# Performance work log

Measured on AMD Instinct MI355X. Metric: run time of the kernel, lower is better.

## Reference

```python
import jax, jax.numpy as jnp
import numpy as np

BEV_H, BEV_W, BEV_Z = 128, 128, 16
N_VOX = BEV_H * BEV_W * BEV_Z  # 262144
C = 128
N_UNMASKED = N_VOX // 4       # 65536 seed voxels (proposal > 0)
LN_EPS = 1e-5
NEG_SLOPE = 0.01


def setup_inputs() -> dict:
    key = jax.random.key(0)
    ks = jax.random.split(key, 8)
    x3d = jax.random.normal(ks[0], (1, C, N_VOX), dtype=jnp.float32)
    # disjoint unmasked/masked index sets from a permutation (proposal mask)
    perm = jax.random.permutation(ks[1], N_VOX)
    unmasked_idx = jnp.sort(perm[:N_UNMASKED]).astype(jnp.int32)
    masked_idx = jnp.sort(perm[N_UNMASKED:]).astype(jnp.int32)
    s = 0.05
    return {
        "x3d": x3d,
        "w1": jax.random.normal(ks[2], (C, C // 2), jnp.float32) * s,
        "b1": jnp.zeros((C // 2,), jnp.float32),
        "ln_g": jnp.ones((C // 2,), jnp.float32),
        "ln_b": jnp.zeros((C // 2,), jnp.float32),
        "w2": jax.random.normal(ks[3], (C // 2, C), jnp.float32) * s,
        "b2": jnp.zeros((C,), jnp.float32),
        "sdb_w": jax.random.normal(ks[4], (C, C // 2), jnp.float32) * s,
        "sdb_b": jnp.zeros((C // 2,), jnp.float32),
        "ssc_w": jax.random.normal(ks[5], (C // 2, 20), jnp.float32) * s,
        "ssc_b": jnp.zeros((20,), jnp.float32),
        "aux_w": jax.random.normal(ks[6], (C, 20), jnp.float32) * s,
        "aux_b": jnp.zeros((20,), jnp.float32),
        "unmasked_idx": unmasked_idx,
        "masked_idx": masked_idx,
    }


def _leaky(x):
    return jnp.where(x > 0, x, NEG_SLOPE * x)


def _layernorm(x, g, b):
    mu = jnp.mean(x, axis=-1, keepdims=True)
    var = jnp.mean(jnp.square(x - mu), axis=-1, keepdims=True)
    return (x - mu) * jax.lax.rsqrt(var + LN_EPS) * g + b


def reference(x3d, w1, b1, ln_g, ln_b, w2, b2, sdb_w, sdb_b, ssc_w, ssc_b,
              aux_w, aux_b, unmasked_idx, masked_idx):
    feats = x3d[0].T  # [N_vox, C]
    # gather seed (unmasked) voxel features; SGB treated as identity stand-in
    seed_feats = feats[unmasked_idx]            # [Nu, C]
    # gather masked voxel features and infill with mlp_prior:
    # Linear -> LayerNorm -> LeakyReLU -> Linear
    m = feats[masked_idx]                       # [Nm, C]
    h = _leaky(_layernorm(m @ w1 + b1, ln_g, ln_b))
    prior = h @ w2 + b2                         # [Nm, C]
    # scatter both into the dense voxel grid
    vox = jnp.zeros((N_VOX, C), x3d.dtype)
    vox = vox.at[unmasked_idx].set(seed_feats).at[masked_idx].set(prior)
    # SDB dense decode stand-in: pointwise conv C -> C/2 + LeakyReLU
    d = _leaky(vox @ sdb_w + sdb_b)             # [N_vox, C/2]
    # ssc head: per-voxel logits -> [1, 20, H, W, Z]
    ssc = d @ ssc_w + ssc_b                     # [N_vox, 20]
    ssc_logit = ssc.reshape(BEV_H, BEV_W, BEV_Z, 20).transpose(3, 0, 1, 2)[None]
    # aux sparse head on seed features
    sem_logit = seed_feats @ aux_w + aux_b      # [Nu, 20]
    return ssc_logit, sem_logit
```

## Files before the change

kernel.cpp:

```cpp
#include <hip/hip_runtime.h>
#include <hip/hip_bf16.h>


#define NVOX 262144
#define NU   65536
#define NM   196608
#define CIN  128
#define CHALF 64
#define NCLS 20
#define TR   64
#define NBLK_M (NM / TR)
#define NBLK_U (NU / TR)

#define SXS 136
#define SHS 72

#define W1F  0
#define W2F  8192
#define SDBF 16384
#define SSCF 24576
#define AUXF 26624
#define WS_TOT 30720

typedef unsigned short u16;
typedef short    bf16x8 __attribute__((ext_vector_type(8)));
typedef float    f32x4  __attribute__((ext_vector_type(4)));

__device__ __forceinline__ u16 f2b(float f) {
    __hip_bfloat16 h = __float2bfloat16(f);
    return *(u16*)&h;
}

__global__ void prep_weights(const float* __restrict__ w1,  const float* __restrict__ w2,
                             const float* __restrict__ sdbw,const float* __restrict__ sscw,
                             const float* __restrict__ auxw,u16* __restrict__ ws) {
    int i = blockIdx.x * blockDim.x + threadIdx.x;
    const int stride = gridDim.x * blockDim.x;
    for (; i < WS_TOT; i += stride) {
        float v;
        if (i < W2F) {
            int t = i, j = t & 7, lane = (t >> 3) & 63, kc = (t >> 9) & 3, nt = t >> 11;
            int k = kc*32 + (lane >> 4)*8 + j, n = nt*16 + (lane & 15);
            v = w1[k*CHALF + n];
        } else if (i < SDBF) {
            int t = i - W2F, j = t & 7, lane = (t >> 3) & 63, kc = (t >> 9) & 1, nt = t >> 10;
            int k = kc*32 + (lane >> 4)*8 + j, n = nt*16 + (lane & 15);
            v = w2[k*CIN + n];
        } else if (i < SSCF) {
            int t = i - SDBF, j = t & 7, lane = (t >> 3) & 63, kc = (t >> 9) & 3, nt = t >> 11;
            int k = kc*32 + (lane >> 4)*8 + j, n = nt*16 + (lane & 15);
            v = sdbw[k*CHALF + n];
        } else if (i < AUXF) {
            int t = i - SSCF, j = t & 7, lane = (t >> 3) & 63, kc = (t >> 9) & 1, nt = t >> 10;
            int k = kc*32 + (lane >> 4)*8 + j, n = nt*16 + (lane & 15);
            v = (n < NCLS) ? sscw[k*NCLS + n] : 0.f;
        } else {
            int t = i - AUXF, j = t & 7, lane = (t >> 3) & 63, kc = (t >> 9) & 3, nt = t >> 11;
            int k = kc*32 + (lane >> 4)*8 + j, n = nt*16 + (lane & 15);
            v = (n < NCLS) ? auxw[k*NCLS + n] : 0.f;
        }
        ws[i] = f2b(v);
    }
}

__global__ __launch_bounds__(256, 3)
void sgn_mfma(const float* __restrict__ x3d,
              const float* __restrict__ b1,   const float* __restrict__ lng,
              const float* __restrict__ lnb,  const float* __restrict__ bb2,
              const float* __restrict__ sdbb, const float* __restrict__ sscb,
              const float* __restrict__ auxb,
              const int* __restrict__ uidx,   const int* __restrict__ midx,
              const u16* __restrict__ wt,     float* __restrict__ out)
{
    __shared__ __align__(16) u16 sX[TR * SXS];
    __shared__ __align__(16) u16 sH[TR * SHS];
    __shared__ __align__(16) u16 wbuf[8192];
    __shared__ int sN[TR];

    const int tid = threadIdx.x;
    const bool masked = (blockIdx.x < NBLK_M);
    const int p0 = (masked ? (int)blockIdx.x : ((int)blockIdx.x - NBLK_M)) * TR;
    const int* __restrict__ idx = masked ? midx : uidx;

    const int r   = tid & 63;
    const int n_r = idx[p0 + r];
    if (tid < TR) sN[tid] = n_r;

    const int cb = (tid >> 6) * 32;
    float v[32];
    #pragma unroll
    for (int j = 0; j < 32; ++j)
        v[j] = x3d[(size_t)(cb + j) * NVOX + n_r];

    {
        const uint4* src = (const uint4*)(wt + (masked ? W1F : SDBF));
        #pragma unroll
        for (int t = 0; t < 4; ++t)
            ((uint4*)wbuf)[tid + t*256] = src[tid + t*256];
    }

    #pragma unroll
    for (int ch = 0; ch < 4; ++ch) {
        bf16x8 pk;
        #pragma unroll
        for (int j = 0; j < 8; ++j) ((u16*)&pk)[j] = f2b(v[ch*8 + j]);
        *(bf16x8*)&sX[r * SXS + cb + ch*8] = pk;
    }
    __syncthreads();

    const int m0   = (tid >> 6) * 16;
    const int lane = tid & 63;
    const int q    = lane >> 4;
    const int n15  = lane & 15;
    const int kq   = q * 8;

    if (masked) {
        f32x4 acc[4];
        #pragma unroll
        for (int nt = 0; nt < 4; ++nt) {
            const float b = b1[nt*16 + n15];
            acc[nt] = (f32x4){b, b, b, b};
        }
        #pragma unroll
        for (int kc = 0; kc < 4; ++kc) {
            const bf16x8 a = *(const bf16x8*)&sX[(m0 + n15) * SXS + kc*32 + kq];
            #pragma unroll
            for (int nt = 0; nt < 4; ++nt) {
                const bf16x8 b = *(const bf16x8*)&wbuf[((nt*4 + kc)*64 + lane)*8];
                acc[nt] = __builtin_amdgcn_mfma_f32_16x16x32_bf16(a, b, acc[nt], 0, 0, 0);
            }
        }
        {
            float gv[4], ev[4];
            #pragma unroll
            for (int nt = 0; nt < 4; ++nt) { gv[nt] = lng[nt*16 + n15]; ev[nt] = lnb[nt*16 + n15]; }
            #pragma unroll
            for (int reg = 0; reg < 4; ++reg) {
                float s1 = acc[0][reg] + acc[1][reg] + acc[2][reg] + acc[3][reg];
                float s2 = acc[0][reg]*acc[0][reg] + acc[1][reg]*acc[1][reg]
                         + acc[2][reg]*acc[2][reg] + acc[3][reg]*acc[3][reg];
                #pragma unroll
                for (int m = 1; m <= 8; m <<= 1) {
                    s1 += __shfl_xor(s1, m, 64);
                    s2 += __shfl_xor(s2, m, 64);
                }
                const float mu  = s1 * (1.f/64.f);
                const float var = s2 * (1.f/64.f) - mu*mu;
                const float rs  = rsqrtf(var + 1e-5f);
                #pragma unroll
                for (int nt = 0; nt < 4; ++nt) {
                    float h = (acc[nt][reg] - mu) * rs * gv[nt] + ev[nt];
                    h = h > 0.f ? h : 0.01f*h;
                    sH[(m0 + q*4 + reg) * SHS + nt*16 + n15] = f2b(h);
                }
            }
        }
        __syncthreads();

        #pragma unroll
        for (int t = 0; t < 4; ++t)
            ((uint4*)wbuf)[tid + t*256] = ((const uint4*)(wt + W2F))[tid + t*256];
        __syncthreads();

        f32x4 acc2[8];
        #pragma unroll
        for (int nt = 0; nt < 8; ++nt) {
            const float b = bb2[nt*16 + n15];
            acc2[nt] = (f32x4){b, b, b, b};
        }
        #pragma unroll
        for (int kc = 0; kc < 2; ++kc) {
            const bf16x8 a = *(const bf16x8*)&sH[(m0 + n15) * SHS + kc*32 + kq];
            #pragma unroll
            for (int nt = 0; nt < 8; ++nt) {
                const bf16x8 b = *(const bf16x8*)&wbuf[((nt*2 + kc)*64 + lane)*8];
                acc2[nt] = __builtin_amdgcn_mfma_f32_16x16x32_bf16(a, b, acc2[nt], 0, 0, 0);
            }
        }
        #pragma unroll
        for (int reg = 0; reg < 4; ++reg)
            #pragma unroll
            for (int nt = 0; nt < 8; ++nt)
                sX[(m0 + q*4 + reg) * SXS + nt*16 + n15] = f2b(acc2[nt][reg]);
        __syncthreads();

        #pragma unroll
        for (int t = 0; t < 4; ++t)
            ((uint4*)wbuf)[tid + t*256] = ((const uint4*)(wt + SDBF))[tid + t*256];
        __syncthreads();
    }

    {
        f32x4 accd[4];
        #pragma unroll
        for (int nt = 0; nt < 4; ++nt) {
            const float b = sdbb[nt*16 + n15];
            accd[nt] = (f32x4){b, b, b, b};
        }
        #pragma unroll
        for (int kc = 0; kc < 4; ++kc) {
            const bf16x8 a = *(const bf16x8*)&sX[(m0 + n15) * SXS + kc*32 + kq];
            #pragma unroll
            for (int nt = 0; nt < 4; ++nt) {
                const bf16x8 b = *(const bf16x8*)&wbuf[((nt*4 + kc)*64 + lane)*8];
                accd[nt] = __builtin_amdgcn_mfma_f32_16x16x32_bf16(a, b, accd[nt], 0, 0, 0);
            }
        }
        #pragma unroll
        for (int reg = 0; reg < 4; ++reg)
            #pragma unroll
            for (int nt = 0; nt < 4; ++nt) {
                float vv = accd[nt][reg];
                vv = vv > 0.f ? vv : 0.01f*vv;
                sH[(m0 + q*4 + reg) * SHS + nt*16 + n15] = f2b(vv);
            }
    }
    __syncthreads();

    if (masked) {
        if (tid < 256) ((uint4*)wbuf)[tid] = ((const uint4*)(wt + SSCF))[tid];
    } else {
        #pragma unroll
        for (int t = 0; t < 3; ++t)
            ((uint4*)wbuf)[tid + t*256] = ((const uint4*)(wt + SSCF))[tid + t*256];
    }
    __syncthreads();

    {
        f32x4 accs[2];
        #pragma unroll
        for (int nt = 0; nt < 2; ++nt) {
            const int col = nt*16 + n15;
            const float b = (col < NCLS) ? sscb[col] : 0.f;
            accs[nt] = (f32x4){b, b, b, b};
        }
        #pragma unroll
        for (int kc = 0; kc < 2; ++kc) {
            const bf16x8 a = *(const bf16x8*)&sH[(m0 + n15) * SHS + kc*32 + kq];
            #pragma unroll
            for (int nt = 0; nt < 2; ++nt) {
                const bf16x8 b = *(const bf16x8*)&wbuf[((nt*2 + kc)*64 + lane)*8];
                accs[nt] = __builtin_amdgcn_mfma_f32_16x16x32_bf16(a, b, accs[nt], 0, 0, 0);
            }
        }
        int ng[4];
        #pragma unroll
        for (int reg = 0; reg < 4; ++reg) ng[reg] = sN[m0 + q*4 + reg];
        #pragma unroll
        for (int reg = 0; reg < 4; ++reg)
            out[(size_t)n15 * NVOX + ng[reg]] = accs[0][reg];
        if (n15 < 4) {
            #pragma unroll
            for (int reg = 0; reg < 4; ++reg)
                out[(size_t)(16 + n15) * NVOX + ng[reg]] = accs[1][reg];
        }
    }

    if (!masked) {
        f32x4 acca[2];
        #pragma unroll
        for (int nt = 0; nt < 2; ++nt) {
            const int col = nt*16 + n15;
            const float b = (col < NCLS) ? auxb[col] : 0.f;
            acca[nt] = (f32x4){b, b, b, b};
        }
        #pragma unroll
        for (int kc = 0; kc < 4; ++kc) {
            const bf16x8 a = *(const bf16x8*)&sX[(m0 + n15) * SXS + kc*32 + kq];
            #pragma unroll
            for (int nt = 0; nt < 2; ++nt) {
                const bf16x8 b = *(const bf16x8*)&wbuf[2048 + ((nt*4 + kc)*64 + lane)*8];
                acca[nt] = __builtin_amdgcn_mfma_f32_16x16x32_bf16(a, b, acca[nt], 0, 0, 0);
            }
        }
        const size_t base = (size_t)NCLS * NVOX;
        #pragma unroll
        for (int reg = 0; reg < 4; ++reg) {
            const int u = p0 + m0 + q*4 + reg;
            out[base + (size_t)u * NCLS + n15] = acca[0][reg];
            if (n15 < 4)
                out[base + (size_t)u * NCLS + 16 + n15] = acca[1][reg];
        }
    }
}

extern "C" void kernel_launch(void* const* d_in, const int* in_sizes, int n_in,
                              void* d_out, int out_size, void* d_ws, size_t ws_size,
                              hipStream_t stream) {
    const float* x3d  = (const float*)d_in[0];
    const float* w1   = (const float*)d_in[1];
    const float* b1   = (const float*)d_in[2];
    const float* lng  = (const float*)d_in[3];
    const float* lnb  = (const float*)d_in[4];
    const float* w2   = (const float*)d_in[5];
    const float* bb2  = (const float*)d_in[6];
    const float* sdbw = (const float*)d_in[7];
    const float* sdbb = (const float*)d_in[8];
    const float* sscw = (const float*)d_in[9];
    const float* sscb = (const float*)d_in[10];
    const float* auxw = (const float*)d_in[11];
    const float* auxb = (const float*)d_in[12];
    const int*   uidx = (const int*)d_in[13];
    const int*   midx = (const int*)d_in[14];
    float* out = (float*)d_out;
    u16*   wt  = (u16*)d_ws;

    hipLaunchKernelGGL(prep_weights, dim3(64), dim3(256), 0, stream,
                       w1, w2, sdbw, sscw, auxw, wt);
    hipLaunchKernelGGL(sgn_mfma, dim3(NBLK_M + NBLK_U), dim3(256), 0, stream,
                       x3d, b1, lng, lnb, bb2, sdbb, sscb, auxb,
                       uidx, midx, wt, out);
}
```

Measured before the change: 263.9 us.

## Process voxels in grid order with a rank map instead of gathering by index

Instead of gathering masked and unmasked voxels through index lists, which makes every x3d read and ssc write strided, each block now takes 64 consecutive voxels. A rank map built in the prep kernel marks each voxel as a seed (its rank) or masked (-1). All voxels run the prior MLP and only masked rows overwrite their features. ssc outputs go through shared memory for coalesced stores. This trades extra MLP and aux compute on every voxel, plus a rank scatter in prep, for fully coalesced vectorized global loads and stores.

```diff
diff --git a/kernel.cpp b/kernel.cpp
--- a/kernel.cpp
+++ b/kernel.cpp
@@ -9,8 +9,7 @@
 #define CHALF 64
 #define NCLS 20
 #define TR   64
-#define NBLK_M (NM / TR)
-#define NBLK_U (NU / TR)
+#define NBLK (NVOX / TR)
 
 #define SXS 136
 #define SHS 72
@@ -20,7 +19,7 @@
 #define SDBF 16384
 #define SSCF 24576
 #define AUXF 26624
-#define WS_TOT 30720
+#define WS_WT 30720
 
 typedef unsigned short u16;
 typedef short    bf16x8 __attribute__((ext_vector_type(8)));
@@ -33,10 +32,15 @@
 
 __global__ void prep_weights(const float* __restrict__ w1,  const float* __restrict__ w2,
                              const float* __restrict__ sdbw,const float* __restrict__ sscw,
-                             const float* __restrict__ auxw,u16* __restrict__ ws) {
+                             const float* __restrict__ auxw,
+                             const int* __restrict__ uidx,  const int* __restrict__ midx,
+                             u16* __restrict__ ws) {
     int i = blockIdx.x * blockDim.x + threadIdx.x;
     const int stride = gridDim.x * blockDim.x;
-    for (; i < WS_TOT; i += stride) {
+    int* __restrict__ rank = (int*)(ws + WS_WT);
+    for (int t = i; t < NU; t += stride) rank[uidx[t]] = t;
+    for (int t = i; t < NM; t += stride) rank[midx[t]] = -1;
+    for (; i < WS_WT; i += stride) {
         float v;
         if (i < W2F) {
             int t = i, j = t & 7, lane = (t >> 3) & 63, kc = (t >> 9) & 3, nt = t >> 11;
@@ -69,42 +73,44 @@
               const float* __restrict__ lnb,  const float* __restrict__ bb2,
               const float* __restrict__ sdbb, const float* __restrict__ sscb,
               const float* __restrict__ auxb,
-              const int* __restrict__ uidx,   const int* __restrict__ midx,
-              const u16* __restrict__ wt,     float* __restrict__ out)
+              const int* __restrict__ rank,   const u16* __restrict__ wt,
+              float* __restrict__ out)
 {
     __shared__ __align__(16) u16 sX[TR * SXS];
     __shared__ __align__(16) u16 sH[TR * SHS];
-    __shared__ __align__(16) u16 wbuf[8192];
-    __shared__ int sN[TR];
+    __shared__ __align__(16) u16 wbuf[8704];
+    __shared__ int sRank[TR];
 
     const int tid = threadIdx.x;
-    const bool masked = (blockIdx.x < NBLK_M);
-    const int p0 = (masked ? (int)blockIdx.x : ((int)blockIdx.x - NBLK_M)) * TR;
-    const int* __restrict__ idx = masked ? midx : uidx;
-
-    const int r   = tid & 63;
-    const int n_r = idx[p0 + r];
-    if (tid < TR) sN[tid] = n_r;
-
-    const int cb = (tid >> 6) * 32;
-    float v[32];
-    #pragma unroll
-    for (int j = 0; j < 32; ++j)
-        v[j] = x3d[(size_t)(cb + j) * NVOX + n_r];
-
-    {
-        const uint4* src = (const uint4*)(wt + (masked ? W1F : SDBF));
+    const int p0  = (int)blockIdx.x * TR;
+
+    const int g  = tid >> 4;
+    const int v0 = (tid & 15) * 4;
+    f32x4 va[4], vb[4];
+    #pragma unroll
+    for (int i = 0; i < 4; ++i) {
+        const int c0 = i*32 + g*2;
+        va[i] = *(const f32x4*)&x3d[(size_t)c0      * NVOX + p0 + v0];
+        vb[i] = *(const f32x4*)&x3d[(size_t)(c0+1)  * NVOX + p0 + v0];
+    }
+
+    if (tid < TR) sRank[tid] = rank[p0 + tid];
+
+    {
+        const uint4* src = (const uint4*)(wt + W1F);
         #pragma unroll
         for (int t = 0; t < 4; ++t)
             ((uint4*)wbuf)[tid + t*256] = src[tid + t*256];
     }
 
     #pragma unroll
-    for (int ch = 0; ch < 4; ++ch) {
-        bf16x8 pk;
-        #pragma unroll
-        for (int j = 0; j < 8; ++j) ((u16*)&pk)[j] = f2b(v[ch*8 + j]);
-        *(bf16x8*)&sX[r * SXS + cb + ch*8] = pk;
+    for (int i = 0; i < 4; ++i) {
+        const int c0 = i*32 + g*2;
+        #pragma unroll
+        for (int j = 0; j < 4; ++j) {
+            unsigned pk = (unsigned)f2b(va[i][j]) | ((unsigned)f2b(vb[i][j]) << 16);
+            *(unsigned*)&sX[(v0 + j)*SXS + c0] = pk;
+        }
     }
     __syncthreads();
 
@@ -114,7 +120,7 @@
     const int n15  = lane & 15;
     const int kq   = q * 8;
 
-    if (masked) {
+    {
         f32x4 acc[4];
         #pragma unroll
         for (int nt = 0; nt < 4; ++nt) {
@@ -130,38 +136,38 @@
                 acc[nt] = __builtin_amdgcn_mfma_f32_16x16x32_bf16(a, b, acc[nt], 0, 0, 0);
             }
         }
-        {
-            float gv[4], ev[4];
-            #pragma unroll
-            for (int nt = 0; nt < 4; ++nt) { gv[nt] = lng[nt*16 + n15]; ev[nt] = lnb[nt*16 + n15]; }
-            #pragma unroll
-            for (int reg = 0; reg < 4; ++reg) {
-                float s1 = acc[0][reg] + acc[1][reg] + acc[2][reg] + acc[3][reg];
-                float s2 = acc[0][reg]*acc[0][reg] + acc[1][reg]*acc[1][reg]
-                         + acc[2][reg]*acc[2][reg] + acc[3][reg]*acc[3][reg];
-                #pragma unroll
-                for (int m = 1; m <= 8; m <<= 1) {
-                    s1 += __shfl_xor(s1, m, 64);
-                    s2 += __shfl_xor(s2, m, 64);
-                }
-                const float mu  = s1 * (1.f/64.f);
-                const float var = s2 * (1.f/64.f) - mu*mu;
-                const float rs  = rsqrtf(var + 1e-5f);
-                #pragma unroll
-                for (int nt = 0; nt < 4; ++nt) {
-                    float h = (acc[nt][reg] - mu) * rs * gv[nt] + ev[nt];
-                    h = h > 0.f ? h : 0.01f*h;
-                    sH[(m0 + q*4 + reg) * SHS + nt*16 + n15] = f2b(h);
-                }
-            }
-        }
-        __syncthreads();
-
-        #pragma unroll
-        for (int t = 0; t < 4; ++t)
-            ((uint4*)wbuf)[tid + t*256] = ((const uint4*)(wt + W2F))[tid + t*256];
-        __syncthreads();
-
+        float gv[4], ev[4];
+        #pragma unroll
+        for (int nt = 0; nt < 4; ++nt) { gv[nt] = lng[nt*16 + n15]; ev[nt] = lnb[nt*16 + n15]; }
+        #pragma unroll
+        for (int reg = 0; reg < 4; ++reg) {
+            float s1 = acc[0][reg] + acc[1][reg] + acc[2][reg] + acc[3][reg];
+            float s2 = acc[0][reg]*acc[0][reg] + acc[1][reg]*acc[1][reg]
+                     + acc[2][reg]*acc[2][reg] + acc[3][reg]*acc[3][reg];
+            #pragma unroll
+            for (int m = 1; m <= 8; m <<= 1) {
+                s1 += __shfl_xor(s1, m, 64);
+                s2 += __shfl_xor(s2, m, 64);
+            }
+            const float mu  = s1 * (1.f/64.f);
+            const float var = s2 * (1.f/64.f) - mu*mu;
+            const float rs  = rsqrtf(var + 1e-5f);
+            #pragma unroll
+            for (int nt = 0; nt < 4; ++nt) {
+                float h = (acc[nt][reg] - mu) * rs * gv[nt] + ev[nt];
+                h = h > 0.f ? h : 0.01f*h;
+                sH[(m0 + q*4 + reg) * SHS + nt*16 + n15] = f2b(h);
+            }
+        }
+    }
+    __syncthreads();
+
+    #pragma unroll
+    for (int t = 0; t < 4; ++t)
+        ((uint4*)wbuf)[tid + t*256] = ((const uint4*)(wt + W2F))[tid + t*256];
+    __syncthreads();
+
+    {
         f32x4 acc2[8];
         #pragma unroll
         for (int nt = 0; nt < 8; ++nt) {
@@ -178,17 +184,21 @@
             }
         }
         #pragma unroll
-        for (int reg = 0; reg < 4; ++reg)
-            #pragma unroll
-            for (int nt = 0; nt < 8; ++nt)
-                sX[(m0 + q*4 + reg) * SXS + nt*16 + n15] = f2b(acc2[nt][reg]);
-        __syncthreads();
-
-        #pragma unroll
-        for (int t = 0; t < 4; ++t)
-            ((uint4*)wbuf)[tid + t*256] = ((const uint4*)(wt + SDBF))[tid + t*256];
-        __syncthreads();
-    }
+        for (int reg = 0; reg < 4; ++reg) {
+            const int row = m0 + q*4 + reg;
+            if (sRank[row] < 0) {
+                #pragma unroll
+                for (int nt = 0; nt < 8; ++nt)
+                    sX[row * SXS + nt*16 + n15] = f2b(acc2[nt][reg]);
+            }
+        }
+    }
+    __syncthreads();
+
+    #pragma unroll
+    for (int t = 0; t < 4; ++t)
+        ((uint4*)wbuf)[tid + t*256] = ((const uint4*)(wt + SDBF))[tid + t*256];
+    __syncthreads();
 
     {
         f32x4 accd[4];
@@ -217,14 +227,12 @@
     }
     __syncthreads();
 
-    if (masked) {
-        if (tid < 256) ((uint4*)wbuf)[tid] = ((const uint4*)(wt + SSCF))[tid];
-    } else {
-        #pragma unroll
-        for (int t = 0; t < 3; ++t)
-            ((uint4*)wbuf)[tid + t*256] = ((const uint4*)(wt + SSCF))[tid + t*256];
-    }
-    __syncthreads();
+    #pragma unroll
+    for (int t = 0; t < 3; ++t)
+        ((uint4*)wbuf)[tid + t*256] = ((const uint4*)(wt + SSCF))[tid + t*256];
+    __syncthreads();
+
+    float* sOut = (float*)(wbuf + 6144);
 
     {
         f32x4 accs[2];
@@ -243,21 +251,16 @@
                 accs[nt] = __builtin_amdgcn_mfma_f32_16x16x32_bf16(a, b, accs[nt], 0, 0, 0);
             }
         }
-        int ng[4];
-        #pragma unroll
-        for (int reg = 0; reg < 4; ++reg) ng[reg] = sN[m0 + q*4 + reg];
-        #pragma unroll
-        for (int reg = 0; reg < 4; ++reg)
-            out[(size_t)n15 * NVOX + ng[reg]] = accs[0][reg];
-        if (n15 < 4) {
-            #pragma unroll
-            for (int reg = 0; reg < 4; ++reg)
-                out[(size_t)(16 + n15) * NVOX + ng[reg]] = accs[1][reg];
-        }
-    }
-
-    if (!masked) {
-        f32x4 acca[2];
+        #pragma unroll
+        for (int reg = 0; reg < 4; ++reg) {
+            const int row = m0 + q*4 + reg;
+            sOut[row*NCLS + n15] = accs[0][reg];
+            if (n15 < 4) sOut[row*NCLS + 16 + n15] = accs[1][reg];
+        }
+    }
+
+    f32x4 acca[2];
+    {
         #pragma unroll
         for (int nt = 0; nt < 2; ++nt) {
             const int col = nt*16 + n15;
@@ -273,13 +276,26 @@
                 acca[nt] = __builtin_amdgcn_mfma_f32_16x16x32_bf16(a, b, acca[nt], 0, 0, 0);
             }
         }
+    }
+    __syncthreads();
+
+    #pragma unroll
+    for (int jj = 0; jj < 5; ++jj) {
+        const int i = tid + jj*256;
+        out[(size_t)(i >> 6) * NVOX + p0 + (i & 63)] = sOut[(i & 63) * NCLS + (i >> 6)];
+    }
+
+    {
         const size_t base = (size_t)NCLS * NVOX;
         #pragma unroll
         for (int reg = 0; reg < 4; ++reg) {
-            const int u = p0 + m0 + q*4 + reg;
-            out[base + (size_t)u * NCLS + n15] = acca[0][reg];
-            if (n15 < 4)
-                out[base + (size_t)u * NCLS + 16 + n15] = acca[1][reg];
+            const int row = m0 + q*4 + reg;
+            const int rk  = sRank[row];
+            if (rk >= 0) {
+                out[base + (size_t)rk * NCLS + n15] = acca[0][reg];
+                if (n15 < 4)
+                    out[base + (size_t)rk * NCLS + 16 + n15] = acca[1][reg];
+            }
         }
     }
 }
@@ -304,10 +320,11 @@
     const int*   midx = (const int*)d_in[14];
     float* out = (float*)d_out;
     u16*   wt  = (u16*)d_ws;
-
-    hipLaunchKernelGGL(prep_weights, dim3(64), dim3(256), 0, stream,
-                       w1, w2, sdbw, sscw, auxw, wt);
-    hipLaunchKernelGGL(sgn_mfma, dim3(NBLK_M + NBLK_U), dim3(256), 0, stream,
+    const int* rank = (const int*)((const char*)d_ws + WS_WT*2);
+
+    hipLaunchKernelGGL(prep_weights, dim3(128), dim3(256), 0, stream,
+                       w1, w2, sdbw, sscw, auxw, uidx, midx, wt);
+    hipLaunchKernelGGL(sgn_mfma, dim3(NBLK), dim3(256), 0, stream,
                        x3d, b1, lng, lnb, bb2, sdbb, sscb, auxb,
-                       uidx, midx, wt, out);
+                       rank, wt, out);
 }
```

After: 249.9 us. 1.06x faster.
